# Kernel optimization log

Measured on AMD Instinct MI355X. Metric: run time of the kernel, lower is better.

The kernel has to match this reference:

```python
import jax, jax.numpy as jnp
import numpy as np

N, M, D = 1024, 32, 512
EPS = 1e-6


def setup_inputs() -> dict:
    key = jax.random.key(0)
    k1, = jax.random.split(key, 1)
    dvecs = jax.random.normal(k1, (N, M, D), dtype=jnp.float32)
    w = jnp.float32(10.0)
    b = jnp.float32(-5.0)
    return {"dvecs": dvecs, "w": w, "b": b}


def reference(dvecs, w, b):
    # dvecs: (N, M, D)
    n, m, d = dvecs.shape
    centroids = dvecs.mean(axis=1)                     # (N, D) full centroids
    # leave-one-out centroid for the reference utterance's own speaker
    c_loo = (dvecs.sum(axis=1, keepdims=True) - dvecs) / (m - 1)   # (N, M, D)

    e_norm = jnp.linalg.norm(dvecs, axis=-1)           # (N, M)
    c_norm = jnp.linalg.norm(centroids, axis=-1)       # (N,)
    c_loo_norm = jnp.linalg.norm(c_loo, axis=-1)       # (N, M)

    # cosine sim against all full centroids: (N, M, N)
    cos = jnp.einsum('jmd,kd->jmk', dvecs, centroids) / (
        e_norm[:, :, None] * c_norm[None, None, :])
    # replace the own-speaker entry with leave-one-out cosine
    loo_cos = jnp.einsum('jmd,jmd->jm', dvecs, c_loo) / (e_norm * c_loo_norm)
    jidx = jnp.arange(n)
    midx = jnp.arange(m)
    cos = cos.at[jidx[:, None], midx[None, :], jidx[:, None]].set(loo_cos)

    # torch.clamp(x, 1e-6) clamps the minimum only
    cos = jnp.maximum(cos, EPS) * w + b

    # softmax embed loss: L[j,i] = -log_softmax(cos[j,i,:])[j]
    logp = jax.nn.log_softmax(cos, axis=-1)
    L = -logp[jidx[:, None], midx[None, :], jidx[:, None]]
    return L.sum()
```

## Files before the change

kernel.cpp:

```cpp
#include <hip/hip_runtime.h>
#include <hip/hip_bf16.h>

#define NSPK 1024
#define MU 32
#define DIM 512
#define DIMP (DIM + 8)
#define NROW (NSPK * MU)
#define EPS 1e-6f

typedef __attribute__((ext_vector_type(4))) float f32x4;
typedef __attribute__((ext_vector_type(8))) short bf16x8;

#define GLOAD_LDS16(g, l)                                          \
  __builtin_amdgcn_global_load_lds(                                \
      (const __attribute__((address_space(1))) void*)(g),          \
      (__attribute__((address_space(3))) void*)(l), 16, 0, 0)

__device__ inline ushort f2bf(float x) {
  __hip_bfloat16 h = __float2bfloat16(x);
  return *reinterpret_cast<ushort*>(&h);
}

__global__ __launch_bounds__(256) void k_prep(
    const float* __restrict__ dvecs,
    ushort* __restrict__ Af,
    ushort* __restrict__ Bf,
    float* __restrict__ loo)
{
  const int j = blockIdx.x, t = threadIdx.x;
  __shared__ float sD[MU * DIMP];
  __shared__ float sS[DIM];
  __shared__ float sred[4];
  __shared__ float sS2v;
  __shared__ float sInv[MU];

  const float* base = dvecs + (size_t)j * (MU * DIM);

  float s0 = 0.f, s1 = 0.f;
  for (int m = 0; m < MU; ++m) {
    float a = base[m * DIM + t];
    float b = base[m * DIM + t + 256];
    sD[m * DIMP + t] = a;
    sD[m * DIMP + t + 256] = b;
    s0 += a; s1 += b;
  }
  sS[t] = s0; sS[t + 256] = s1;
  __syncthreads();

  float p = s0 * s0 + s1 * s1;
  for (int off = 32; off; off >>= 1) p += __shfl_down(p, off);
  if ((t & 63) == 0) sred[t >> 6] = p;
  __syncthreads();
  if (t == 0) sS2v = sred[0] + sred[1] + sred[2] + sred[3];
  __syncthreads();
  const float S2 = sS2v;

  const int g = t >> 3, l = t & 7;
  float dotS = 0.f, e2 = 0.f;
  for (int i = 0; i < DIM / 8; ++i) {
    int d = i * 8 + l;
    float ev = sD[g * DIMP + d];
    dotS += ev * sS[d];
    e2 += ev * ev;
  }
  for (int off = 4; off; off >>= 1) {
    dotS += __shfl_down(dotS, off);
    e2 += __shfl_down(e2, off);
  }
  if (l == 0) {
    float numer = dotS - e2;
    float d2 = fmaxf(S2 - 2.f * dotS + e2, 1e-30f);
    loo[j * MU + g] = numer / (sqrtf(e2) * sqrtf(d2));
    sInv[g] = 1.f / sqrtf(e2);
  }
  __syncthreads();

  for (int i = 0; i < 8; ++i) {
    int idx = i * 256 + t;
    int fragL = idx >> 6;
    int lane2 = idx & 63;
    int rbl = fragL >> 4, kf = fragL & 15;
    int m = rbl * 16 + (lane2 & 15);
    int k0 = kf * 32 + (lane2 >> 4) * 8;
    float inv = sInv[m];
    ushort tmp[8];
#pragma unroll
    for (int z = 0; z < 8; ++z) tmp[z] = f2bf(sD[m * DIMP + k0 + z] * inv);
    *(bf16x8*)&Af[(((size_t)(j * 2 + rbl) * 16 + kf) << 9) + lane2 * 8] =
        *(bf16x8*)tmp;
  }

  if (t < 64) {
    int kf = t >> 2, q = t & 3;
    int lane2 = q * 16 + (j & 15);
    float invc = 1.f / sqrtf(S2);
    int k0 = kf * 32 + q * 8;
    ushort tmp[8];
#pragma unroll
    for (int z = 0; z < 8; ++z) tmp[z] = f2bf(sS[k0 + z] * invc);
    *(bf16x8*)&Bf[(((size_t)(j >> 4) * 16 + kf) << 9) + lane2 * 8] =
        *(bf16x8*)tmp;
  }
}

__global__ __launch_bounds__(256, 1) void k_gemm(
    const ushort* __restrict__ Af,
    const ushort* __restrict__ Bf,
    const float* __restrict__ wp,
    float* __restrict__ part,
    float* __restrict__ diag)
{
  __shared__ ushort ldsA[3 * 8 * 512];
  __shared__ ushort ldsB[3 * 8 * 512];
  __shared__ float sPart[128][2];

  const int t = threadIdx.x;
  const int w = t >> 6, lane = t & 63;
  const int lr = lane & 15, lk = lane >> 4;
  const int wm = w >> 1, wn = w & 1;
  const int bid = blockIdx.x;
  const int xcd = bid & 7, ii = bid >> 3;
  const int rb = xcd * 32 + (ii >> 3);
  const int cb = ii & 7;

  f32x4 acc[4][4];
#pragma unroll
  for (int a = 0; a < 4; ++a)
#pragma unroll
    for (int b = 0; b < 4; ++b) acc[a][b] = (f32x4)0.f;

  const ushort* gA0 = Af + (((size_t)(rb * 8 + w) * 16) << 9) + lane * 8;
  const ushort* gA1 = Af + (((size_t)(rb * 8 + w + 4) * 16) << 9) + lane * 8;
  const ushort* gB0 = Bf + (((size_t)(cb * 8 + w) * 16) << 9) + lane * 8;
  const ushort* gB1 = Bf + (((size_t)(cb * 8 + w + 4) * 16) << 9) + lane * 8;
  ushort* dA0 = &ldsA[w * 512 + lane * 8];
  ushort* dA1 = &ldsA[(w + 4) * 512 + lane * 8];
  ushort* dB0 = &ldsB[w * 512 + lane * 8];
  ushort* dB1 = &ldsB[(w + 4) * 512 + lane * 8];

#define STAGE(kt, bi)                                   \
  {                                                     \
    GLOAD_LDS16(gA0 + (kt) * 512, dA0 + (bi) * 4096);   \
    GLOAD_LDS16(gA1 + (kt) * 512, dA1 + (bi) * 4096);   \
    GLOAD_LDS16(gB0 + (kt) * 512, dB0 + (bi) * 4096);   \
    GLOAD_LDS16(gB1 + (kt) * 512, dB1 + (bi) * 4096);   \
  }

  bf16x8 afr[2][4], bfr[2][4];
  const ushort* lA0 = &ldsA[(wm * 4) * 512 + lane * 8];
  const ushort* lB0 = &ldsB[(wn * 4) * 512 + lane * 8];

#define DSREAD(set, bi)                                                   \
  {                                                                       \
    _Pragma("unroll")                                                     \
    for (int nf = 0; nf < 4; ++nf)                                        \
      bfr[set][nf] = *(const bf16x8*)(lB0 + (bi) * 4096 + nf * 512);      \
    _Pragma("unroll")                                                     \
    for (int mf = 0; mf < 4; ++mf)                                        \
      afr[set][mf] = *(const bf16x8*)(lA0 + (bi) * 4096 + mf * 512);      \
  }

  STAGE(0, 0);
  STAGE(1, 1);
  asm volatile("s_waitcnt vmcnt(4)" ::: "memory");
  __builtin_amdgcn_s_barrier();
  __builtin_amdgcn_sched_barrier(0);
  STAGE(2, 2);
  DSREAD(0, 0);
  asm volatile("s_waitcnt lgkmcnt(0)" ::: "memory");
  __builtin_amdgcn_sched_barrier(0);

#pragma unroll
  for (int kt = 0; kt < 16; ++kt) {
    if (kt < 14) {
      asm volatile("s_waitcnt vmcnt(4)" ::: "memory");
    } else {
      asm volatile("s_waitcnt vmcnt(0)" ::: "memory");
    }
    __builtin_amdgcn_s_barrier();
    __builtin_amdgcn_sched_barrier(0);

    if (kt <= 12) STAGE(kt + 3, (kt + 3) % 3);
    if (kt < 15) DSREAD((kt + 1) & 1, (kt + 1) % 3);

    __builtin_amdgcn_s_setprio(1);
#pragma unroll
    for (int mf = 0; mf < 4; ++mf)
#pragma unroll
      for (int nf = 0; nf < 4; ++nf)
        acc[mf][nf] = __builtin_amdgcn_mfma_f32_16x16x32_bf16(
            afr[kt & 1][mf], bfr[kt & 1][nf], acc[mf][nf], 0, 0, 0);
    __builtin_amdgcn_s_setprio(0);

    if (kt < 15) {
      asm volatile("s_waitcnt lgkmcnt(0)" ::: "memory");
      __builtin_amdgcn_sched_barrier(0);
    }
  }
#undef STAGE
#undef DSREAD

  const float W = *wp;

  if (cb == (rb >> 5)) {
#pragma unroll
    for (int sp = 0; sp < 4; ++sp) {
      const int c = rb * 4 + sp;
      if (wm == (sp >> 1) && wn == ((c >> 6) & 1)) {
        const int nfo = (c >> 4) & 3;
#pragma unroll
        for (int mh = 0; mh < 2; ++mh) {
          f32x4 dsel = acc[(sp & 1) * 2 + mh][0];
#pragma unroll
          for (int nf = 1; nf < 4; ++nf)
            if (nf == nfo) dsel = acc[(sp & 1) * 2 + mh][nf];
          if (lr == (c & 15)) {
#pragma unroll
            for (int i = 0; i < 4; ++i)
              diag[c * 32 + mh * 16 + lk * 4 + i] = dsel[i];
          }
        }
      }
    }
  }

#pragma unroll
  for (int mf = 0; mf < 4; ++mf)
#pragma unroll
    for (int i = 0; i < 4; ++i) {
      float s = 0.f;
#pragma unroll
      for (int nf = 0; nf < 4; ++nf)
        s += __expf((fmaxf(acc[mf][nf][i], EPS) - 1.f) * W);
      s += __shfl_xor(s, 1);
      s += __shfl_xor(s, 2);
      s += __shfl_xor(s, 4);
      s += __shfl_xor(s, 8);
      if (lr == 0) sPart[wm * 64 + mf * 16 + lk * 4 + i][wn] = s;
    }
  __syncthreads();
  if (t < 128)
    part[(size_t)cb * NROW + rb * 128 + t] = sPart[t][0] + sPart[t][1];
}

__global__ __launch_bounds__(256) void k_final1(
    const float* __restrict__ part, const float* __restrict__ loo,
    const float* __restrict__ diag, const float* __restrict__ wp,
    float* __restrict__ p2)
{
  const int t = threadIdx.x;
  const int r = blockIdx.x * 256 + t;
  const float W = *wp;
  float s = 0.f;
#pragma unroll
  for (int c = 0; c < 8; ++c) s += part[(size_t)c * NROW + r];
  const float lt = (fmaxf(loo[r], EPS) - 1.f) * W;
  const float dt = (fmaxf(diag[r], EPS) - 1.f) * W;
  s += __expf(lt) - __expf(dt);
  float v = logf(s) - lt;
  __shared__ float red[4];
  for (int off = 32; off; off >>= 1) v += __shfl_down(v, off);
  if ((t & 63) == 0) red[t >> 6] = v;
  __syncthreads();
  if (t == 0) p2[blockIdx.x] = red[0] + red[1] + red[2] + red[3];
}

__global__ __launch_bounds__(128) void k_final2(
    const float* __restrict__ p2, float* __restrict__ out)
{
  const int t = threadIdx.x;
  float v = p2[t];
  for (int off = 32; off; off >>= 1) v += __shfl_down(v, off);
  __shared__ float red[2];
  if ((t & 63) == 0) red[t >> 6] = v;
  __syncthreads();
  if (t == 0) out[0] = red[0] + red[1];
}

extern "C" void kernel_launch(void* const* d_in, const int* in_sizes, int n_in,
                              void* d_out, int out_size, void* d_ws, size_t ws_size,
                              hipStream_t stream) {
  const float* dvecs = (const float*)d_in[0];
  const float* wptr  = (const float*)d_in[1];
  float* out = (float*)d_out;

  char* ws = (char*)d_ws;
  ushort* Af = (ushort*)ws;  ws += (size_t)NROW * DIM * sizeof(ushort);
  ushort* Bf = (ushort*)ws;  ws += (size_t)NSPK * DIM * sizeof(ushort);
  float* loo  = (float*)ws;  ws += (size_t)NROW * sizeof(float);
  float* diag = (float*)ws;  ws += (size_t)NROW * sizeof(float);
  float* part = (float*)ws;  ws += (size_t)8 * NROW * sizeof(float);
  float* p2   = (float*)ws;

  k_prep<<<NSPK, 256, 0, stream>>>(dvecs, Af, Bf, loo);
  k_gemm<<<2048, 256, 0, stream>>>(Af, Bf, wptr, part, diag);
  k_final1<<<NROW / 256, 256, 0, stream>>>(part, loo, diag, wptr, p2);
  k_final2<<<1, 128, 0, stream>>>(p2, out);
}
```

Measured before the change: 69.09 us.

## Widen GEMM column tile to 256 and simplify LDS read pipeline

Doubles the k_gemm output tile width from 128 to 256 columns per block, so each wave accumulates 4x8 MFMA fragments and the grid halves to 1024 blocks, which reduces how often the A operand is reloaded. The prefetch depth drops from three stages ahead to two, and LDS fragment reads are no longer double-buffered across iterations; each iteration now reads its fragments right before the MFMAs. The partial-sum buffer and final reduction now use 4 column chunks instead of 8. The cost is higher register and LDS use, lost overlap between LDS reads and MFMA, and fewer blocks to fill the CUs.

```diff
diff --git a/kernel.cpp b/kernel.cpp
--- a/kernel.cpp
+++ b/kernel.cpp
@@ -111,7 +111,7 @@
     float* __restrict__ diag)
 {
   __shared__ ushort ldsA[3 * 8 * 512];
-  __shared__ ushort ldsB[3 * 8 * 512];
+  __shared__ ushort ldsB[3 * 16 * 512];
   __shared__ float sPart[128][2];
 
   const int t = threadIdx.x;
@@ -120,76 +120,73 @@
   const int wm = w >> 1, wn = w & 1;
   const int bid = blockIdx.x;
   const int xcd = bid & 7, ii = bid >> 3;
-  const int rb = xcd * 32 + (ii >> 3);
-  const int cb = ii & 7;
-
-  f32x4 acc[4][4];
+  const int rb = xcd * 32 + (ii >> 2);
+  const int cb = ii & 3;
+
+  f32x4 acc[4][8];
 #pragma unroll
   for (int a = 0; a < 4; ++a)
 #pragma unroll
-    for (int b = 0; b < 4; ++b) acc[a][b] = (f32x4)0.f;
+    for (int b = 0; b < 8; ++b) acc[a][b] = (f32x4)0.f;
 
   const ushort* gA0 = Af + (((size_t)(rb * 8 + w) * 16) << 9) + lane * 8;
   const ushort* gA1 = Af + (((size_t)(rb * 8 + w + 4) * 16) << 9) + lane * 8;
-  const ushort* gB0 = Bf + (((size_t)(cb * 8 + w) * 16) << 9) + lane * 8;
-  const ushort* gB1 = Bf + (((size_t)(cb * 8 + w + 4) * 16) << 9) + lane * 8;
+  const ushort* gB0 = Bf + (((size_t)(cb * 16 + w) * 16) << 9) + lane * 8;
+  const ushort* gB1 = Bf + (((size_t)(cb * 16 + w + 4) * 16) << 9) + lane * 8;
+  const ushort* gB2 = Bf + (((size_t)(cb * 16 + w + 8) * 16) << 9) + lane * 8;
+  const ushort* gB3 = Bf + (((size_t)(cb * 16 + w + 12) * 16) << 9) + lane * 8;
   ushort* dA0 = &ldsA[w * 512 + lane * 8];
   ushort* dA1 = &ldsA[(w + 4) * 512 + lane * 8];
   ushort* dB0 = &ldsB[w * 512 + lane * 8];
   ushort* dB1 = &ldsB[(w + 4) * 512 + lane * 8];
+  ushort* dB2 = &ldsB[(w + 8) * 512 + lane * 8];
+  ushort* dB3 = &ldsB[(w + 12) * 512 + lane * 8];
 
 #define STAGE(kt, bi)                                   \
   {                                                     \
     GLOAD_LDS16(gA0 + (kt) * 512, dA0 + (bi) * 4096);   \
     GLOAD_LDS16(gA1 + (kt) * 512, dA1 + (bi) * 4096);   \
-    GLOAD_LDS16(gB0 + (kt) * 512, dB0 + (bi) * 4096);   \
-    GLOAD_LDS16(gB1 + (kt) * 512, dB1 + (bi) * 4096);   \
-  }
-
-  bf16x8 afr[2][4], bfr[2][4];
+    GLOAD_LDS16(gB0 + (kt) * 512, dB0 + (bi) * 8192);   \
+    GLOAD_LDS16(gB1 + (kt) * 512, dB1 + (bi) * 8192);   \
+    GLOAD_LDS16(gB2 + (kt) * 512, dB2 + (bi) * 8192);   \
+    GLOAD_LDS16(gB3 + (kt) * 512, dB3 + (bi) * 8192);   \
+  }
+
   const ushort* lA0 = &ldsA[(wm * 4) * 512 + lane * 8];
-  const ushort* lB0 = &ldsB[(wn * 4) * 512 + lane * 8];
-
-#define DSREAD(set, bi)                                                   \
-  {                                                                       \
-    _Pragma("unroll")                                                     \
-    for (int nf = 0; nf < 4; ++nf)                                        \
-      bfr[set][nf] = *(const bf16x8*)(lB0 + (bi) * 4096 + nf * 512);      \
-    _Pragma("unroll")                                                     \
-    for (int mf = 0; mf < 4; ++mf)                                        \
-      afr[set][mf] = *(const bf16x8*)(lA0 + (bi) * 4096 + mf * 512);      \
-  }
+  const ushort* lB0 = &ldsB[(wn * 8) * 512 + lane * 8];
 
   STAGE(0, 0);
   STAGE(1, 1);
-  asm volatile("s_waitcnt vmcnt(4)" ::: "memory");
-  __builtin_amdgcn_s_barrier();
-  __builtin_amdgcn_sched_barrier(0);
-  STAGE(2, 2);
-  DSREAD(0, 0);
-  asm volatile("s_waitcnt lgkmcnt(0)" ::: "memory");
-  __builtin_amdgcn_sched_barrier(0);
 
 #pragma unroll
   for (int kt = 0; kt < 16; ++kt) {
-    if (kt < 14) {
-      asm volatile("s_waitcnt vmcnt(4)" ::: "memory");
+    if (kt < 15) {
+      asm volatile("s_waitcnt vmcnt(6)" ::: "memory");
     } else {
       asm volatile("s_waitcnt vmcnt(0)" ::: "memory");
     }
     __builtin_amdgcn_s_barrier();
     __builtin_amdgcn_sched_barrier(0);
 
-    if (kt <= 12) STAGE(kt + 3, (kt + 3) % 3);
-    if (kt < 15) DSREAD((kt + 1) & 1, (kt + 1) % 3);
+    if (kt <= 13) STAGE(kt + 2, (kt + 2) % 3);
+
+    const ushort* lA = lA0 + (kt % 3) * 4096;
+    const ushort* lB = lB0 + (kt % 3) * 8192;
+    bf16x8 afr[4], bfr[8];
+#pragma unroll
+    for (int nf = 0; nf < 8; ++nf)
+      bfr[nf] = *(const bf16x8*)(lB + nf * 512);
+#pragma unroll
+    for (int mf = 0; mf < 4; ++mf)
+      afr[mf] = *(const bf16x8*)(lA + mf * 512);
 
     __builtin_amdgcn_s_setprio(1);
 #pragma unroll
     for (int mf = 0; mf < 4; ++mf)
 #pragma unroll
-      for (int nf = 0; nf < 4; ++nf)
+      for (int nf = 0; nf < 8; ++nf)
         acc[mf][nf] = __builtin_amdgcn_mfma_f32_16x16x32_bf16(
-            afr[kt & 1][mf], bfr[kt & 1][nf], acc[mf][nf], 0, 0, 0);
+            afr[mf], bfr[nf], acc[mf][nf], 0, 0, 0);
     __builtin_amdgcn_s_setprio(0);
 
     if (kt < 15) {
@@ -198,21 +195,20 @@
     }
   }
 #undef STAGE
-#undef DSREAD
 
   const float W = *wp;
 
-  if (cb == (rb >> 5)) {
+  if (cb == (rb >> 6)) {
 #pragma unroll
     for (int sp = 0; sp < 4; ++sp) {
       const int c = rb * 4 + sp;
-      if (wm == (sp >> 1) && wn == ((c >> 6) & 1)) {
-        const int nfo = (c >> 4) & 3;
+      if (wm == (sp >> 1) && wn == ((c >> 7) & 1)) {
+        const int nfo = (c >> 4) & 7;
 #pragma unroll
         for (int mh = 0; mh < 2; ++mh) {
           f32x4 dsel = acc[(sp & 1) * 2 + mh][0];
 #pragma unroll
-          for (int nf = 1; nf < 4; ++nf)
+          for (int nf = 1; nf < 8; ++nf)
             if (nf == nfo) dsel = acc[(sp & 1) * 2 + mh][nf];
           if (lr == (c & 15)) {
 #pragma unroll
@@ -230,7 +226,7 @@
     for (int i = 0; i < 4; ++i) {
       float s = 0.f;
 #pragma unroll
-      for (int nf = 0; nf < 4; ++nf)
+      for (int nf = 0; nf < 8; ++nf)
         s += __expf((fmaxf(acc[mf][nf][i], EPS) - 1.f) * W);
       s += __shfl_xor(s, 1);
       s += __shfl_xor(s, 2);
@@ -253,7 +249,7 @@
   const float W = *wp;
   float s = 0.f;
 #pragma unroll
-  for (int c = 0; c < 8; ++c) s += part[(size_t)c * NROW + r];
+  for (int c = 0; c < 4; ++c) s += part[(size_t)c * NROW + r];
   const float lt = (fmaxf(loo[r], EPS) - 1.f) * W;
   const float dt = (fmaxf(diag[r], EPS) - 1.f) * W;
   s += __expf(lt) - __expf(dt);
@@ -289,11 +285,11 @@
   ushort* Bf = (ushort*)ws;  ws += (size_t)NSPK * DIM * sizeof(ushort);
   float* loo  = (float*)ws;  ws += (size_t)NROW * sizeof(float);
   float* diag = (float*)ws;  ws += (size_t)NROW * sizeof(float);
-  float* part = (float*)ws;  ws += (size_t)8 * NROW * sizeof(float);
+  float* part = (float*)ws;  ws += (size_t)4 * NROW * sizeof(float);
   float* p2   = (float*)ws;
 
   k_prep<<<NSPK, 256, 0, stream>>>(dvecs, Af, Bf, loo);
-  k_gemm<<<2048, 256, 0, stream>>>(Af, Bf, wptr, part, diag);
+  k_gemm<<<1024, 256, 0, stream>>>(Af, Bf, wptr, part, diag);
   k_final1<<<NROW / 256, 256, 0, stream>>>(part, loo, diag, wptr, p2);
   k_final2<<<1, 128, 0, stream>>>(p2, out);
 }
```

Result: slower. 89.24 us (+29.2%).
